# Kernel optimization log

Measured on AMD Instinct MI355X. Metric: run time of the kernel, lower is better.

The kernel has to match this reference:

```python
import jax, jax.numpy as jnp
import numpy as np

GAMMA = 10.0          # entropy_regularizer_weight
N_ITERS = 10          # optimization_steps
EPS = np.float32(7.0 / 3 - 4.0 / 3 - 1.0)  # matches tf.constant(7/3-4/3-1, float32)

B, W, H, D = 128, 28, 28, 512
S = 128               # support_size


def setup_inputs() -> dict:
    key = jax.random.key(0)
    k1, k2 = jax.random.split(key)
    features = jax.random.normal(k1, (B, W, H, D), dtype=jnp.float32)
    # GlorotUniform-like init for the target support (learned codebook)
    limit = np.sqrt(6.0 / (S + D)).astype(np.float32)
    target_support = jax.random.uniform(k2, (S, D), dtype=jnp.float32,
                                        minval=-limit, maxval=limit)
    return {"features": features, "target_support": target_support}


def _l2norm(x):
    return x / jnp.sqrt(jnp.sum(x * x, axis=-1, keepdims=True))


def reference(features, target_support):
    b, w, h, d = features.shape
    s = target_support.shape[0]
    n = w * h  # num_feats

    t = _l2norm(target_support)                 # (S, D)
    f = _l2norm(features).reshape(b, n, d)      # (B, N, D)

    # pairwise squared L2 distance between normalized vectors: 2 - 2*cos
    c = 2.0 - 2.0 * jnp.einsum('sd,bnd->bsn', t, f)  # (B, S, N)

    K = jnp.exp(-GAMMA * c)                     # (B, S, N)
    q = jnp.full((1, 1, n), 1.0 / n, dtype=jnp.float32)  # marginal over feats
    p = jnp.full((1, 1, s), 1.0 / s, dtype=jnp.float32)  # marginal over support

    u = jnp.ones((b, 1, s), dtype=jnp.float32)
    Kt = jnp.swapaxes(K, 1, 2)                  # (B, N, S)
    for _ in range(N_ITERS):
        v = q / (jnp.matmul(u, K) + EPS)        # (B, 1, N)
        u = p / (jnp.matmul(v, Kt) + EPS)       # (B, 1, S)
    v = q / (jnp.matmul(u, K) + EPS)

    # transport plan Pi = u^T * K * v  -> (B, S, N)
    Pi = jnp.swapaxes(u, 1, 2) * K * v
    return Pi
```

## Files before the change

### kernel.cpp

```cpp
#include <hip/hip_runtime.h>
#include <hip/hip_fp16.h>

#define EPS_C   2.2204460492503131e-16f
#define NS      128
#define ND      512
#define NN      784
#define NB      128
#define BSN     (NS*NN)
#define QM      (1.0f/784.0f)
#define LOG2E20 28.853900817779268f

typedef __attribute__((ext_vector_type(8))) short bf16x8;
typedef __attribute__((ext_vector_type(4))) float f32x4;

static __device__ __forceinline__ ushort f2bf(float x) {
    uint u = __float_as_uint(x);
    uint r = (u + 0x7FFFu + ((u >> 16) & 1u)) >> 16;
    return (ushort)r;
}
static __device__ __forceinline__ float bf2f(ushort h) {
    return __uint_as_float(((uint)h) << 16);
}
static __device__ __forceinline__ uint cvtpk_bf16(float a, float b) {
    uint r;
    asm("v_cvt_pk_bf16_f32 %0, %1, %2" : "=v"(r) : "v"(a), "v"(b));
    return r;
}

__global__ __launch_bounds__(128)
void tnorm_kernel(const float* __restrict__ t,
                  ushort* __restrict__ tnh, ushort* __restrict__ tnl) {
    int s = blockIdx.x, tid = threadIdx.x;
    float4 x = ((const float4*)(t + s * ND))[tid];
    float ss = x.x*x.x + x.y*x.y + x.z*x.z + x.w*x.w;
#pragma unroll
    for (int off = 1; off < 64; off <<= 1) ss += __shfl_xor(ss, off);
    __shared__ float red[2];
    if ((tid & 63) == 0) red[tid >> 6] = ss;
    __syncthreads();
    float rs = 1.0f / sqrtf(red[0] + red[1]);
    float y[4] = {x.x*rs, x.y*rs, x.z*rs, x.w*rs};
    ushort h[4], l[4];
#pragma unroll
    for (int k = 0; k < 4; k++) {
        h[k] = f2bf(y[k]);
        l[k] = f2bf(y[k] - bf2f(h[k]));
    }
    *(ushort4*)(tnh + s * ND + tid * 4) = make_ushort4(h[0], h[1], h[2], h[3]);
    *(ushort4*)(tnl + s * ND + tid * 4) = make_ushort4(l[0], l[1], l[2], l[3]);
}

#define LDK 40

__global__ void __launch_bounds__(256)
__attribute__((amdgpu_waves_per_eu(2, 4)))
gemm_k_kernel(const ushort* __restrict__ Ahi, const ushort* __restrict__ Alo,
              const float* __restrict__ f, uint* __restrict__ Kp) {
    __shared__ ushort Bsh[2][NS * LDK];
    __shared__ float  ssq_sh[128];

    const int tid  = threadIdx.x;
    const int lane = tid & 63;
    const int wid  = tid >> 6;
    const int wm   = wid & 1;
    const int wn   = wid >> 1;
    const int j0   = blockIdx.x * 128;

    const int brow  = tid >> 3;
    const int bcol4 = (tid & 7) * 4;

    const float* bPtr[4];
#pragma unroll
    for (int p = 0; p < 4; p++)
        bPtr[p] = f + (size_t)(j0 + p * 32 + brow) * ND + bcol4;

    const int mrow = lane & 15;
    const int koff = (lane >> 4) * 8;

    const ushort* aPtrH[4];
    const ushort* aPtrL[4];
#pragma unroll
    for (int i = 0; i < 4; i++) {
        int r = wm * 64 + i * 16 + mrow;
        aPtrH[i] = Ahi + (size_t)r * ND + koff;
        aPtrL[i] = Alo + (size_t)r * ND + koff;
    }

    f32x4 acc[4][4];
#pragma unroll
    for (int i = 0; i < 4; i++)
#pragma unroll
        for (int j = 0; j < 4; j++) acc[i][j] = (f32x4){0.f, 0.f, 0.f, 0.f};
    float ssqp[4] = {0.f, 0.f, 0.f, 0.f};

    float4 bReg[4];
#pragma unroll
    for (int p = 0; p < 4; p++) bReg[p] = *(const float4*)bPtr[p];

    for (int d0 = 0; d0 < ND; d0 += 32) {
        bf16x8 ah[4], al[4];
#pragma unroll
        for (int i = 0; i < 4; i++) ah[i] = *(const bf16x8*)(aPtrH[i] + d0);
#pragma unroll
        for (int i = 0; i < 4; i++) al[i] = *(const bf16x8*)(aPtrL[i] + d0);

#pragma unroll
        for (int p = 0; p < 4; p++) {
            float4 v = bReg[p];
            ssqp[p] += v.x*v.x + v.y*v.y + v.z*v.z + v.w*v.w;
            uint hA = cvtpk_bf16(v.x, v.y);
            uint hB = cvtpk_bf16(v.z, v.w);
            float rx = v.x - __uint_as_float(hA << 16);
            float ry = v.y - __uint_as_float(hA & 0xFFFF0000u);
            float rz = v.z - __uint_as_float(hB << 16);
            float rw = v.w - __uint_as_float(hB & 0xFFFF0000u);
            uint lA = cvtpk_bf16(rx, ry);
            uint lB = cvtpk_bf16(rz, rw);
            int c = p * 32 + brow;
            *(uint2*)&Bsh[0][c * LDK + bcol4] = make_uint2(hA, hB);
            *(uint2*)&Bsh[1][c * LDK + bcol4] = make_uint2(lA, lB);
        }
        __syncthreads();
        if (d0 + 32 < ND) {
#pragma unroll
            for (int p = 0; p < 4; p++)
                bReg[p] = *(const float4*)(bPtr[p] + d0 + 32);
        }
        bf16x8 bb[4];
#pragma unroll
        for (int j = 0; j < 4; j++)
            bb[j] = *(const bf16x8*)&Bsh[0][(wn*64 + j*16 + mrow) * LDK + koff];
#pragma unroll
        for (int i = 0; i < 4; i++)
#pragma unroll
            for (int j = 0; j < 4; j++)
                acc[i][j] = __builtin_amdgcn_mfma_f32_16x16x32_bf16(ah[i], bb[j], acc[i][j], 0, 0, 0);
#pragma unroll
        for (int i = 0; i < 4; i++)
#pragma unroll
            for (int j = 0; j < 4; j++)
                acc[i][j] = __builtin_amdgcn_mfma_f32_16x16x32_bf16(al[i], bb[j], acc[i][j], 0, 0, 0);
#pragma unroll
        for (int j = 0; j < 4; j++)
            bb[j] = *(const bf16x8*)&Bsh[1][(wn*64 + j*16 + mrow) * LDK + koff];
#pragma unroll
        for (int i = 0; i < 4; i++)
#pragma unroll
            for (int j = 0; j < 4; j++)
                acc[i][j] = __builtin_amdgcn_mfma_f32_16x16x32_bf16(ah[i], bb[j], acc[i][j], 0, 0, 0);
        __syncthreads();
    }

#pragma unroll
    for (int p = 0; p < 4; p++) {
#pragma unroll
        for (int off = 1; off < 8; off <<= 1) ssqp[p] += __shfl_xor(ssqp[p], off);
    }
    if ((tid & 7) == 0) {
#pragma unroll
        for (int p = 0; p < 4; p++) ssq_sh[p * 32 + (tid >> 3)] = ssqp[p];
    }
    __syncthreads();

    const int quad4 = (lane >> 4) << 2;
#pragma unroll
    for (int jt = 0; jt < 4; jt++) {
        int cloc = wn * 64 + jt * 16 + mrow;
        float rq = rsqrtf(ssq_sh[cloc]) * LOG2E20;
        int jg = j0 + cloc;
        int b2 = jg / NN;
        int nn = jg - b2 * NN;
        int jj = nn >> 6, l = nn & 63;
#pragma unroll
        for (int i = 0; i < 4; i++) {
            int s0 = wm * 64 + i * 16 + quad4;
            float k0 = exp2f(acc[i][jt][0] * rq);
            float k1 = exp2f(acc[i][jt][1] * rq);
            float k2v = exp2f(acc[i][jt][2] * rq);
            float k3 = exp2f(acc[i][jt][3] * rq);
            __half2 lo = __halves2half2(__float2half(k0), __float2half(k1));
            __half2 hi = __halves2half2(__float2half(k2v), __float2half(k3));
            size_t dw = (((size_t)(b2 * 16 + (s0 >> 3)) * 13 + jj) * 64 + l) * 4
                        + ((s0 & 7) >> 1);
            *(uint2*)(Kp + dw) = make_uint2(__builtin_bit_cast(uint, lo),
                                            __builtin_bit_cast(uint, hi));
        }
    }
}

#define VSCALE 64.0f
#define PM64   (VSCALE/128.0f)
#define EPS64  (EPS_C*VSCALE)

__global__ void __launch_bounds__(1024)
__attribute__((amdgpu_waves_per_eu(4, 4)))
sinkhorn_kernel(const uint* __restrict__ Kp, float* __restrict__ Pi) {
    __shared__ float slab[16 * NN];
    __shared__ float v_sh[NN];
    const int b    = blockIdx.x;
    const int tid  = threadIdx.x;
    const int lane = tid & 63;
    const int w    = tid >> 6;
    float* Pib = Pi + (size_t)b * BSN;

    const uint4* kbase = (const uint4*)Kp + (size_t)(b * 16 + w) * 13 * 64 + lane;
    __half2 k2[13][4];
#pragma unroll
    for (int j = 0; j < 13; j++) {
        uint4 t = kbase[j * 64];
        k2[j][0] = __builtin_bit_cast(__half2, t.x);
        k2[j][1] = __builtin_bit_cast(__half2, t.y);
        k2[j][2] = __builtin_bit_cast(__half2, t.z);
        k2[j][3] = __builtin_bit_cast(__half2, t.w);
    }
    if (lane >= 16) {
#pragma unroll
        for (int rp = 0; rp < 4; rp++) k2[12][rp] = __halves2half2(__half(0.f), __half(0.f));
    }

    __half2 u2[4];
    float uf[8];
#pragma unroll
    for (int rp = 0; rp < 4; rp++) u2[rp] = __halves2half2(__half(1.f), __half(1.f));
#pragma unroll
    for (int r = 0; r < 8; r++) uf[r] = 1.f;

    float* myrow = &slab[w * NN];

    for (int it = 0; it <= 10; ++it) {
#pragma unroll
        for (int j = 0; j < 13; j++) {
            int n = lane + (j << 6);
            float pa = 0.f;
#pragma unroll
            for (int rp = 0; rp < 4; rp++)
                pa = __builtin_amdgcn_fdot2(k2[j][rp], u2[rp], pa, false);
            if (n < NN) myrow[n] = pa;
        }
        __syncthreads();
        if (tid < NN) {
            float s0 = 0.f, s1 = 0.f, s2 = 0.f, s3 = 0.f;
#pragma unroll
            for (int w2 = 0; w2 < 16; w2 += 4) {
                s0 += slab[(w2 + 0) * NN + tid];
                s1 += slab[(w2 + 1) * NN + tid];
                s2 += slab[(w2 + 2) * NN + tid];
                s3 += slab[(w2 + 3) * NN + tid];
            }
            v_sh[tid] = QM / (((s0 + s1) + (s2 + s3)) + EPS_C);
        }
        __syncthreads();
        if (it == 10) break;
        __half2 acc2[4];
#pragma unroll
        for (int rp = 0; rp < 4; rp++) acc2[rp] = __halves2half2(__half(0.f), __half(0.f));
#pragma unroll
        for (int j = 0; j < 13; j++) {
            int n = lane + (j << 6);
            int ni = (n < NN) ? n : 0;
            float vv = v_sh[ni] * VSCALE;
            __half vh = __float2half(vv);
            __half2 vh2 = __halves2half2(vh, vh);
#pragma unroll
            for (int rp = 0; rp < 4; rp++)
                acc2[rp] = __hfma2(vh2, k2[j][rp], acc2[rp]);
        }
#pragma unroll
        for (int rp = 0; rp < 4; rp++) {
#pragma unroll
            for (int off = 1; off < 64; off <<= 1) {
                int y = __shfl_xor(__builtin_bit_cast(int, acc2[rp]), off);
                acc2[rp] = __hadd2(acc2[rp], __builtin_bit_cast(__half2, y));
            }
            float2 af = __half22float2(acc2[rp]);
            uf[2*rp]     = PM64 / (af.x + EPS64);
            uf[2*rp + 1] = PM64 / (af.y + EPS64);
            u2[rp] = __halves2half2(__float2half(uf[2*rp]), __float2half(uf[2*rp+1]));
        }
    }

#pragma unroll
    for (int j = 0; j < 13; j++) {
        int n = lane + (j << 6);
        if (n < NN) {
            float vv = v_sh[n];
#pragma unroll
            for (int rp = 0; rp < 4; rp++) {
                float2 kk = __half22float2(k2[j][rp]);
                Pib[(size_t)(8*w + 2*rp    ) * NN + n] = uf[2*rp]     * kk.x * vv;
                Pib[(size_t)(8*w + 2*rp + 1) * NN + n] = uf[2*rp + 1] * kk.y * vv;
            }
        }
    }
}

extern "C" void kernel_launch(void* const* d_in, const int* in_sizes, int n_in,
                              void* d_out, int out_size, void* d_ws, size_t ws_size,
                              hipStream_t stream) {
    const float* feat = (const float*)d_in[0];
    const float* tsup = (const float*)d_in[1];
    float* out = (float*)d_out;

    ushort* tnh = (ushort*)d_ws;
    ushort* tnl = tnh + NS * ND;
    uint*   Kp  = (uint*)(tnl + NS * ND);

    tnorm_kernel<<<NS, 128, 0, stream>>>(tsup, tnh, tnl);
    gemm_k_kernel<<<(NB * NN) / 128, 256, 0, stream>>>(tnh, tnl, feat, Kp);
    sinkhorn_kernel<<<NB, 1024, 0, stream>>>(Kp, out);
}
```

Baseline: 357.1 us.

## Load feature B-operand directly into MFMA registers, dropping the LDS staging

The GEMM kernel no longer stages the fp32 feature tile through shared memory. Each wave now loads the exact 8-float fragments it needs straight into registers, splits them into bf16 hi/lo pairs in registers, and computes the row sum-of-squares with cross-lane shuffles. This removes the LDS writes and reads and both __syncthreads per k-step. In exchange, the two waves sharing a column group each load and convert the same B data, so global loads and conversion work are duplicated, and register pressure rises, hence the waves_per_eu limit is tightened to (2,2).

```diff
diff --git a/kernel.cpp b/kernel.cpp
--- a/kernel.cpp
+++ b/kernel.cpp
@@ -12,6 +12,7 @@
 
 typedef __attribute__((ext_vector_type(8))) short bf16x8;
 typedef __attribute__((ext_vector_type(4))) float f32x4;
+typedef __attribute__((ext_vector_type(8))) float f32x8;
 
 static __device__ __forceinline__ ushort f2bf(float x) {
     uint u = __float_as_uint(x);
@@ -50,15 +51,10 @@
     *(ushort4*)(tnl + s * ND + tid * 4) = make_ushort4(l[0], l[1], l[2], l[3]);
 }
 
-#define LDK 40
-
 __global__ void __launch_bounds__(256)
-__attribute__((amdgpu_waves_per_eu(2, 4)))
+__attribute__((amdgpu_waves_per_eu(2, 2)))
 gemm_k_kernel(const ushort* __restrict__ Ahi, const ushort* __restrict__ Alo,
               const float* __restrict__ f, uint* __restrict__ Kp) {
-    __shared__ ushort Bsh[2][NS * LDK];
-    __shared__ float  ssq_sh[128];
-
     const int tid  = threadIdx.x;
     const int lane = tid & 63;
     const int wid  = tid >> 6;
@@ -66,14 +62,6 @@
     const int wn   = wid >> 1;
     const int j0   = blockIdx.x * 128;
 
-    const int brow  = tid >> 3;
-    const int bcol4 = (tid & 7) * 4;
-
-    const float* bPtr[4];
-#pragma unroll
-    for (int p = 0; p < 4; p++)
-        bPtr[p] = f + (size_t)(j0 + p * 32 + brow) * ND + bcol4;
-
     const int mrow = lane & 15;
     const int koff = (lane >> 4) * 8;
 
@@ -85,6 +73,10 @@
         aPtrH[i] = Ahi + (size_t)r * ND + koff;
         aPtrL[i] = Alo + (size_t)r * ND + koff;
     }
+    const float* bPtr[4];
+#pragma unroll
+    for (int j = 0; j < 4; j++)
+        bPtr[j] = f + (size_t)(j0 + wn * 64 + j * 16 + mrow) * ND + koff;
 
     f32x4 acc[4][4];
 #pragma unroll
@@ -93,9 +85,9 @@
         for (int j = 0; j < 4; j++) acc[i][j] = (f32x4){0.f, 0.f, 0.f, 0.f};
     float ssqp[4] = {0.f, 0.f, 0.f, 0.f};
 
-    float4 bReg[4];
-#pragma unroll
-    for (int p = 0; p < 4; p++) bReg[p] = *(const float4*)bPtr[p];
+    f32x8 bF[4];
+#pragma unroll
+    for (int j = 0; j < 4; j++) bF[j] = *(const f32x8*)(bPtr[j]);
 
     for (int d0 = 0; d0 < ND; d0 += 32) {
         bf16x8 ah[4], al[4];
@@ -103,70 +95,71 @@
         for (int i = 0; i < 4; i++) ah[i] = *(const bf16x8*)(aPtrH[i] + d0);
 #pragma unroll
         for (int i = 0; i < 4; i++) al[i] = *(const bf16x8*)(aPtrL[i] + d0);
-
-#pragma unroll
-        for (int p = 0; p < 4; p++) {
-            float4 v = bReg[p];
-            ssqp[p] += v.x*v.x + v.y*v.y + v.z*v.z + v.w*v.w;
-            uint hA = cvtpk_bf16(v.x, v.y);
-            uint hB = cvtpk_bf16(v.z, v.w);
-            float rx = v.x - __uint_as_float(hA << 16);
-            float ry = v.y - __uint_as_float(hA & 0xFFFF0000u);
-            float rz = v.z - __uint_as_float(hB << 16);
-            float rw = v.w - __uint_as_float(hB & 0xFFFF0000u);
-            uint lA = cvtpk_bf16(rx, ry);
-            uint lB = cvtpk_bf16(rz, rw);
-            int c = p * 32 + brow;
-            *(uint2*)&Bsh[0][c * LDK + bcol4] = make_uint2(hA, hB);
-            *(uint2*)&Bsh[1][c * LDK + bcol4] = make_uint2(lA, lB);
-        }
-        __syncthreads();
-        if (d0 + 32 < ND) {
-#pragma unroll
-            for (int p = 0; p < 4; p++)
-                bReg[p] = *(const float4*)(bPtr[p] + d0 + 32);
-        }
-        bf16x8 bb[4];
-#pragma unroll
-        for (int j = 0; j < 4; j++)
-            bb[j] = *(const bf16x8*)&Bsh[0][(wn*64 + j*16 + mrow) * LDK + koff];
+        const bool hasNext = (d0 + 32 < ND);
+        f32x8 bN[4];
+        if (hasNext) {
+#pragma unroll
+            for (int j = 0; j < 4; j++) bN[j] = *(const f32x8*)(bPtr[j] + d0 + 32);
+        }
+        bf16x8 bh[4], bl[4];
+#pragma unroll
+        for (int j = 0; j < 4; j++) {
+            f32x8 v = bF[j];
+            ssqp[j] += v[0]*v[0] + v[1]*v[1] + v[2]*v[2] + v[3]*v[3]
+                     + v[4]*v[4] + v[5]*v[5] + v[6]*v[6] + v[7]*v[7];
+            uint h0 = cvtpk_bf16(v[0], v[1]);
+            uint h1 = cvtpk_bf16(v[2], v[3]);
+            uint h2 = cvtpk_bf16(v[4], v[5]);
+            uint h3 = cvtpk_bf16(v[6], v[7]);
+            float r0 = v[0] - __uint_as_float(h0 << 16);
+            float r1 = v[1] - __uint_as_float(h0 & 0xFFFF0000u);
+            float r2 = v[2] - __uint_as_float(h1 << 16);
+            float r3 = v[3] - __uint_as_float(h1 & 0xFFFF0000u);
+            float r4 = v[4] - __uint_as_float(h2 << 16);
+            float r5 = v[5] - __uint_as_float(h2 & 0xFFFF0000u);
+            float r6 = v[6] - __uint_as_float(h3 << 16);
+            float r7 = v[7] - __uint_as_float(h3 & 0xFFFF0000u);
+            uint l0 = cvtpk_bf16(r0, r1);
+            uint l1 = cvtpk_bf16(r2, r3);
+            uint l2 = cvtpk_bf16(r4, r5);
+            uint l3 = cvtpk_bf16(r6, r7);
+            uint4 hp = make_uint4(h0, h1, h2, h3);
+            uint4 lp = make_uint4(l0, l1, l2, l3);
+            bh[j] = __builtin_bit_cast(bf16x8, hp);
+            bl[j] = __builtin_bit_cast(bf16x8, lp);
+        }
 #pragma unroll
         for (int i = 0; i < 4; i++)
 #pragma unroll
             for (int j = 0; j < 4; j++)
-                acc[i][j] = __builtin_amdgcn_mfma_f32_16x16x32_bf16(ah[i], bb[j], acc[i][j], 0, 0, 0);
+                acc[i][j] = __builtin_amdgcn_mfma_f32_16x16x32_bf16(ah[i], bh[j], acc[i][j], 0, 0, 0);
 #pragma unroll
         for (int i = 0; i < 4; i++)
 #pragma unroll
             for (int j = 0; j < 4; j++)
-                acc[i][j] = __builtin_amdgcn_mfma_f32_16x16x32_bf16(al[i], bb[j], acc[i][j], 0, 0, 0);
-#pragma unroll
-        for (int j = 0; j < 4; j++)
-            bb[j] = *(const bf16x8*)&Bsh[1][(wn*64 + j*16 + mrow) * LDK + koff];
+                acc[i][j] = __builtin_amdgcn_mfma_f32_16x16x32_bf16(al[i], bh[j], acc[i][j], 0, 0, 0);
 #pragma unroll
         for (int i = 0; i < 4; i++)
 #pragma unroll
             for (int j = 0; j < 4; j++)
-                acc[i][j] = __builtin_amdgcn_mfma_f32_16x16x32_bf16(ah[i], bb[j], acc[i][j], 0, 0, 0);
-        __syncthreads();
-    }
-
-#pragma unroll
-    for (int p = 0; p < 4; p++) {
-#pragma unroll
-        for (int off = 1; off < 8; off <<= 1) ssqp[p] += __shfl_xor(ssqp[p], off);
-    }
-    if ((tid & 7) == 0) {
-#pragma unroll
-        for (int p = 0; p < 4; p++) ssq_sh[p * 32 + (tid >> 3)] = ssqp[p];
-    }
-    __syncthreads();
+                acc[i][j] = __builtin_amdgcn_mfma_f32_16x16x32_bf16(ah[i], bl[j], acc[i][j], 0, 0, 0);
+        if (hasNext) {
+#pragma unroll
+            for (int j = 0; j < 4; j++) bF[j] = bN[j];
+        }
+    }
+
+#pragma unroll
+    for (int j = 0; j < 4; j++) {
+        ssqp[j] += __shfl_xor(ssqp[j], 16);
+        ssqp[j] += __shfl_xor(ssqp[j], 32);
+    }
 
     const int quad4 = (lane >> 4) << 2;
 #pragma unroll
     for (int jt = 0; jt < 4; jt++) {
         int cloc = wn * 64 + jt * 16 + mrow;
-        float rq = rsqrtf(ssq_sh[cloc]) * LOG2E20;
+        float rq = rsqrtf(ssqp[jt]) * LOG2E20;
         int jg = j0 + cloc;
         int b2 = jg / NN;
         int nn = jg - b2 * NN;
```

After: 403.3 us. 12.9% more time.

## Split Sinkhorn batch across two cooperating blocks and double-buffer GEMM B tile

Applied to the files above, without the earlier changes.

The Sinkhorn kernel now runs two 512-thread blocks per batch instead of one 1024-thread block, so twice as many workgroups can spread over the CUs. Each block reduces its half of the support rows into a global buffer, then spins on a per-batch flag to combine partial column sums with its partner every iteration. The GEMM kernel also double-buffers the shared B tile, which removes one barrier per K-step and overlaps conversion of the next tile with MFMA work. The spin-wait assumes both partner blocks are resident at once and adds global-memory round trips on every iteration.

```diff
diff --git a/kernel.cpp b/kernel.cpp
--- a/kernel.cpp
+++ b/kernel.cpp
@@ -29,8 +29,10 @@
 
 __global__ __launch_bounds__(128)
 void tnorm_kernel(const float* __restrict__ t,
-                  ushort* __restrict__ tnh, ushort* __restrict__ tnl) {
+                  ushort* __restrict__ tnh, ushort* __restrict__ tnl,
+                  int* __restrict__ flags) {
     int s = blockIdx.x, tid = threadIdx.x;
+    if (tid < 2) flags[2 * s + tid] = 0;
     float4 x = ((const float4*)(t + s * ND))[tid];
     float ss = x.x*x.x + x.y*x.y + x.z*x.z + x.w*x.w;
 #pragma unroll
@@ -56,7 +58,7 @@
 __attribute__((amdgpu_waves_per_eu(2, 4)))
 gemm_k_kernel(const ushort* __restrict__ Ahi, const ushort* __restrict__ Alo,
               const float* __restrict__ f, uint* __restrict__ Kp) {
-    __shared__ ushort Bsh[2][NS * LDK];
+    __shared__ ushort Bsh[2][2][128 * LDK];
     __shared__ float  ssq_sh[128];
 
     const int tid  = threadIdx.x;
@@ -94,9 +96,30 @@
     float ssqp[4] = {0.f, 0.f, 0.f, 0.f};
 
     float4 bReg[4];
+
 #pragma unroll
     for (int p = 0; p < 4; p++) bReg[p] = *(const float4*)bPtr[p];
-
+#pragma unroll
+    for (int p = 0; p < 4; p++) {
+        float4 v = bReg[p];
+        ssqp[p] += v.x*v.x + v.y*v.y + v.z*v.z + v.w*v.w;
+        uint hA = cvtpk_bf16(v.x, v.y);
+        uint hB = cvtpk_bf16(v.z, v.w);
+        float rx = v.x - __uint_as_float(hA << 16);
+        float ry = v.y - __uint_as_float(hA & 0xFFFF0000u);
+        float rz = v.z - __uint_as_float(hB << 16);
+        float rw = v.w - __uint_as_float(hB & 0xFFFF0000u);
+        uint lA = cvtpk_bf16(rx, ry);
+        uint lB = cvtpk_bf16(rz, rw);
+        int c = p * 32 + brow;
+        *(uint2*)&Bsh[0][0][c * LDK + bcol4] = make_uint2(hA, hB);
+        *(uint2*)&Bsh[0][1][c * LDK + bcol4] = make_uint2(lA, lB);
+    }
+#pragma unroll
+    for (int p = 0; p < 4; p++) bReg[p] = *(const float4*)(bPtr[p] + 32);
+    __syncthreads();
+
+    int buf = 0;
     for (int d0 = 0; d0 < ND; d0 += 32) {
         bf16x8 ah[4], al[4];
 #pragma unroll
@@ -104,32 +127,10 @@
 #pragma unroll
         for (int i = 0; i < 4; i++) al[i] = *(const bf16x8*)(aPtrL[i] + d0);
 
-#pragma unroll
-        for (int p = 0; p < 4; p++) {
-            float4 v = bReg[p];
-            ssqp[p] += v.x*v.x + v.y*v.y + v.z*v.z + v.w*v.w;
-            uint hA = cvtpk_bf16(v.x, v.y);
-            uint hB = cvtpk_bf16(v.z, v.w);
-            float rx = v.x - __uint_as_float(hA << 16);
-            float ry = v.y - __uint_as_float(hA & 0xFFFF0000u);
-            float rz = v.z - __uint_as_float(hB << 16);
-            float rw = v.w - __uint_as_float(hB & 0xFFFF0000u);
-            uint lA = cvtpk_bf16(rx, ry);
-            uint lB = cvtpk_bf16(rz, rw);
-            int c = p * 32 + brow;
-            *(uint2*)&Bsh[0][c * LDK + bcol4] = make_uint2(hA, hB);
-            *(uint2*)&Bsh[1][c * LDK + bcol4] = make_uint2(lA, lB);
-        }
-        __syncthreads();
-        if (d0 + 32 < ND) {
-#pragma unroll
-            for (int p = 0; p < 4; p++)
-                bReg[p] = *(const float4*)(bPtr[p] + d0 + 32);
-        }
         bf16x8 bb[4];
 #pragma unroll
         for (int j = 0; j < 4; j++)
-            bb[j] = *(const bf16x8*)&Bsh[0][(wn*64 + j*16 + mrow) * LDK + koff];
+            bb[j] = *(const bf16x8*)&Bsh[buf][0][(wn*64 + j*16 + mrow) * LDK + koff];
 #pragma unroll
         for (int i = 0; i < 4; i++)
 #pragma unroll
@@ -142,13 +143,37 @@
                 acc[i][j] = __builtin_amdgcn_mfma_f32_16x16x32_bf16(al[i], bb[j], acc[i][j], 0, 0, 0);
 #pragma unroll
         for (int j = 0; j < 4; j++)
-            bb[j] = *(const bf16x8*)&Bsh[1][(wn*64 + j*16 + mrow) * LDK + koff];
+            bb[j] = *(const bf16x8*)&Bsh[buf][1][(wn*64 + j*16 + mrow) * LDK + koff];
 #pragma unroll
         for (int i = 0; i < 4; i++)
 #pragma unroll
             for (int j = 0; j < 4; j++)
                 acc[i][j] = __builtin_amdgcn_mfma_f32_16x16x32_bf16(ah[i], bb[j], acc[i][j], 0, 0, 0);
-        __syncthreads();
+
+        if (d0 + 32 < ND) {
+#pragma unroll
+            for (int p = 0; p < 4; p++) {
+                float4 v = bReg[p];
+                ssqp[p] += v.x*v.x + v.y*v.y + v.z*v.z + v.w*v.w;
+                uint hA = cvtpk_bf16(v.x, v.y);
+                uint hB = cvtpk_bf16(v.z, v.w);
+                float rx = v.x - __uint_as_float(hA << 16);
+                float ry = v.y - __uint_as_float(hA & 0xFFFF0000u);
+                float rz = v.z - __uint_as_float(hB << 16);
+                float rw = v.w - __uint_as_float(hB & 0xFFFF0000u);
+                uint lA = cvtpk_bf16(rx, ry);
+                uint lB = cvtpk_bf16(rz, rw);
+                int c = p * 32 + brow;
+                *(uint2*)&Bsh[buf^1][0][c * LDK + bcol4] = make_uint2(hA, hB);
+                *(uint2*)&Bsh[buf^1][1][c * LDK + bcol4] = make_uint2(lA, lB);
+            }
+        }
+        if (d0 + 64 < ND) {
+#pragma unroll
+            for (int p = 0; p < 4; p++) bReg[p] = *(const float4*)(bPtr[p] + d0 + 64);
+        }
+        __syncthreads();
+        buf ^= 1;
     }
 
 #pragma unroll
@@ -192,18 +217,26 @@
 #define PM64   (VSCALE/128.0f)
 #define EPS64  (EPS_C*VSCALE)
 
-__global__ void __launch_bounds__(1024)
-__attribute__((amdgpu_waves_per_eu(4, 4)))
-sinkhorn_kernel(const uint* __restrict__ Kp, float* __restrict__ Pi) {
-    __shared__ float slab[16 * NN];
+__global__ void __launch_bounds__(512)
+sinkhorn_kernel(const uint* __restrict__ Kp, float* __restrict__ Pi,
+                float* __restrict__ gbuf, int* __restrict__ flags) {
+    __shared__ float slab[8 * NN];
     __shared__ float v_sh[NN];
-    const int b    = blockIdx.x;
+    const int bq   = blockIdx.x;
+    const int b    = bq >> 1;
+    const int q    = bq & 1;
     const int tid  = threadIdx.x;
     const int lane = tid & 63;
     const int w    = tid >> 6;
+    const int wg   = 8 * q + w;
     float* Pib = Pi + (size_t)b * BSN;
 
-    const uint4* kbase = (const uint4*)Kp + (size_t)(b * 16 + w) * 13 * 64 + lane;
+    float* gOwn = gbuf + ((size_t)b * 2 + q)       * (2 * NN);
+    float* gOth = gbuf + ((size_t)b * 2 + (1 - q)) * (2 * NN);
+    int* fOwn = flags + 2 * b + q;
+    int* fOth = flags + 2 * b + (1 - q);
+
+    const uint4* kbase = (const uint4*)Kp + (size_t)(b * 16 + wg) * 13 * 64 + lane;
     __half2 k2[13][4];
 #pragma unroll
     for (int j = 0; j < 13; j++) {
@@ -226,6 +259,8 @@
     for (int r = 0; r < 8; r++) uf[r] = 1.f;
 
     float* myrow = &slab[w * NN];
+    const int n0 = tid;
+    const int n1 = tid + 512;
 
     for (int it = 0; it <= 10; ++it) {
 #pragma unroll
@@ -238,16 +273,41 @@
             if (n < NN) myrow[n] = pa;
         }
         __syncthreads();
-        if (tid < NN) {
-            float s0 = 0.f, s1 = 0.f, s2 = 0.f, s3 = 0.f;
-#pragma unroll
-            for (int w2 = 0; w2 < 16; w2 += 4) {
-                s0 += slab[(w2 + 0) * NN + tid];
-                s1 += slab[(w2 + 1) * NN + tid];
-                s2 += slab[(w2 + 2) * NN + tid];
-                s3 += slab[(w2 + 3) * NN + tid];
-            }
-            v_sh[tid] = QM / (((s0 + s1) + (s2 + s3)) + EPS_C);
+        const int par = it & 1;
+        float own0, own1 = 0.f;
+        {
+            float s0 = slab[0*NN+n0] + slab[1*NN+n0];
+            float s1 = slab[2*NN+n0] + slab[3*NN+n0];
+            float s2 = slab[4*NN+n0] + slab[5*NN+n0];
+            float s3 = slab[6*NN+n0] + slab[7*NN+n0];
+            own0 = (s0 + s1) + (s2 + s3);
+            __hip_atomic_store(&gOwn[par*NN + n0], own0,
+                               __ATOMIC_RELAXED, __HIP_MEMORY_SCOPE_AGENT);
+        }
+        if (n1 < NN) {
+            float s0 = slab[0*NN+n1] + slab[1*NN+n1];
+            float s1 = slab[2*NN+n1] + slab[3*NN+n1];
+            float s2 = slab[4*NN+n1] + slab[5*NN+n1];
+            float s3 = slab[6*NN+n1] + slab[7*NN+n1];
+            own1 = (s0 + s1) + (s2 + s3);
+            __hip_atomic_store(&gOwn[par*NN + n1], own1,
+                               __ATOMIC_RELAXED, __HIP_MEMORY_SCOPE_AGENT);
+        }
+        __syncthreads();
+        if (tid == 0) {
+            __hip_atomic_store(fOwn, it + 1, __ATOMIC_RELEASE, __HIP_MEMORY_SCOPE_AGENT);
+            while (__hip_atomic_load(fOth, __ATOMIC_ACQUIRE, __HIP_MEMORY_SCOPE_AGENT) <= it) {}
+        }
+        __syncthreads();
+        {
+            float tot = own0 + __hip_atomic_load(&gOth[par*NN + n0],
+                                                 __ATOMIC_RELAXED, __HIP_MEMORY_SCOPE_AGENT);
+            v_sh[n0] = QM / (tot + EPS_C);
+        }
+        if (n1 < NN) {
+            float tot = own1 + __hip_atomic_load(&gOth[par*NN + n1],
+                                                 __ATOMIC_RELAXED, __HIP_MEMORY_SCOPE_AGENT);
+            v_sh[n1] = QM / (tot + EPS_C);
         }
         __syncthreads();
         if (it == 10) break;
@@ -287,8 +347,8 @@
 #pragma unroll
             for (int rp = 0; rp < 4; rp++) {
                 float2 kk = __half22float2(k2[j][rp]);
-                Pib[(size_t)(8*w + 2*rp    ) * NN + n] = uf[2*rp]     * kk.x * vv;
-                Pib[(size_t)(8*w + 2*rp + 1) * NN + n] = uf[2*rp + 1] * kk.y * vv;
+                Pib[(size_t)(8*wg + 2*rp    ) * NN + n] = uf[2*rp]     * kk.x * vv;
+                Pib[(size_t)(8*wg + 2*rp + 1) * NN + n] = uf[2*rp + 1] * kk.y * vv;
             }
         }
     }
@@ -301,11 +361,13 @@
     const float* tsup = (const float*)d_in[1];
     float* out = (float*)d_out;
 
-    ushort* tnh = (ushort*)d_ws;
-    ushort* tnl = tnh + NS * ND;
-    uint*   Kp  = (uint*)(tnl + NS * ND);
-
-    tnorm_kernel<<<NS, 128, 0, stream>>>(tsup, tnh, tnl);
+    ushort* tnh   = (ushort*)d_ws;
+    ushort* tnl   = tnh + NS * ND;
+    uint*   Kp    = (uint*)(tnl + NS * ND);
+    float*  gbuf  = (float*)(Kp + (size_t)NB * 16 * 13 * 64 * 4);
+    int*    flags = (int*)(gbuf + (size_t)NB * 2 * 2 * NN);
+
+    tnorm_kernel<<<NS, 128, 0, stream>>>(tsup, tnh, tnl, flags);
     gemm_k_kernel<<<(NB * NN) / 128, 256, 0, stream>>>(tnh, tnl, feat, Kp);
-    sinkhorn_kernel<<<NB, 1024, 0, stream>>>(Kp, out);
-}
+    sinkhorn_kernel<<<NB * 2, 512, 0, stream>>>(Kp, out, gbuf, flags);
+}
```

New measurement: 428.7 us. 20.0% more time.
